# Performance work log

Hardware: AMD Instinct MI355X
Metric: run time of the kernel (lower is better)

The kernel has to match this reference:

```python
import jax, jax.numpy as jnp
import numpy as np

H = 1024
E = 8
TOP_K = 2


def setup_inputs() -> dict:
    key = jax.random.key(0)
    ks = jax.random.split(key, 6)
    B, S = 4, 2048
    hidden_states = jax.random.normal(ks[0], (B, S, H), dtype=jnp.float32)
    # router weight, init N(0, 0.02)
    router_w = jax.random.normal(ks[1], (E, H), dtype=jnp.float32) * 0.02
    # stacked expert FFN params (nn.Linear: y = x @ W.T + b)
    lim = 1.0 / np.sqrt(H)
    W1 = jax.random.uniform(ks[2], (E, H, H), minval=-lim, maxval=lim, dtype=jnp.float32)
    b1 = jax.random.uniform(ks[3], (E, H), minval=-lim, maxval=lim, dtype=jnp.float32)
    W2 = jax.random.uniform(ks[4], (E, H, H), minval=-lim, maxval=lim, dtype=jnp.float32)
    b2 = jax.random.uniform(ks[5], (E, H), minval=-lim, maxval=lim, dtype=jnp.float32)
    return {"hidden_states": hidden_states, "router_w": router_w,
            "W1": W1, "b1": b1, "W2": W2, "b2": b2}


def reference(hidden_states, router_w, W1, b1, W2, b2):
    B, S, _ = hidden_states.shape
    # ---- router ----
    logits = jnp.einsum('bsh,eh->bse', hidden_states, router_w)  # [B,S,E]
    router_probs = jax.nn.softmax(logits.astype(jnp.float32), axis=-1)
    top_vals, top_idx = jax.lax.top_k(router_probs, TOP_K)        # [B,S,K]
    top_vals = top_vals / jnp.sum(top_vals, axis=-1, keepdims=True)  # norm_topk_prob
    # per-token per-expert combine weight (sum of top-k weights matching expert)
    w = jnp.sum(jax.nn.one_hot(top_idx, E, dtype=top_vals.dtype) * top_vals[..., None], axis=-2)  # [B,S,E]
    # ---- dense all-expert FFN (faithful to reference: every expert on every token) ----
    h1 = jax.nn.relu(jnp.einsum('bsh,efh->bsef', hidden_states, W1) + b1)   # [B,S,E,F]
    expert_out = jnp.einsum('bsef,egf->bseg', h1, W2) + b2                  # [B,S,E,H]
    moe_out = jnp.einsum('bseh,bse->bsh', expert_out, w)
    return hidden_states + moe_out, router_probs
```

## Files before the change

kernel.cpp:

```cpp
#include <hip/hip_runtime.h>
#include <hip/hip_bf16.h>


#define HD   1024
#define NTOK 8192
#define NEXP 8
#define BM   128
#define BN   128
#define BK   32
#define ZROW 8192
#define MAXP 17408
#define EP_LDSW 136

typedef __attribute__((ext_vector_type(8))) short  vshort8;
typedef __attribute__((ext_vector_type(4))) short  vshort4;
typedef __attribute__((ext_vector_type(4))) float  vfloat4;

typedef __attribute__((address_space(1))) const unsigned gas_uint;
typedef __attribute__((address_space(3))) unsigned       las_uint;

__device__ __forceinline__ void gld16(const void* g, void* l) {
    __builtin_amdgcn_global_load_lds((gas_uint*)g, (las_uint*)l, 16, 0, 0);
}

__device__ __forceinline__ short bf16r(float f) {
    union { float f; unsigned u; } a; a.f = f;
    unsigned r = a.u + 0x7FFFu + ((a.u >> 16) & 1u);
    return (short)(r >> 16);
}

__global__ void init_kernel(int* counts, int* fill, int* pair_token, short* xb) {
    int i = blockIdx.x * 256 + threadIdx.x;
    if (i < NEXP) { counts[i] = 0; fill[i] = 0; }
    if (i < MAXP) pair_token[i] = ZROW;
    if (i < HD / 8) {
        vshort8 z = {0, 0, 0, 0, 0, 0, 0, 0};
        *(vshort8*)(xb + (size_t)ZROW * HD + i * 8) = z;
    }
}

__global__ __launch_bounds__(256) void router_kernel(
    const float* __restrict__ x, const float* __restrict__ rw,
    float* __restrict__ out, short* __restrict__ xb,
    float* __restrict__ probs_out, int2* __restrict__ tok_top,
    float2* __restrict__ tok_w, int* __restrict__ counts) {
    __shared__ float rws[NEXP * HD];
    __shared__ int hist[NEXP];
    int t = threadIdx.x;
    if (t < NEXP) hist[t] = 0;
    for (int j = 0; j < 8; ++j) {
        int idx = j * 1024 + t * 4;
        *(vfloat4*)(rws + idx) = *(const vfloat4*)(rw + idx);
    }
    __syncthreads();
    int wave = t >> 6, lane = t & 63;
    for (int it = 0; it < 8; ++it) {
        int token = blockIdx.x * 32 + it * 4 + wave;
        const float* xr = x + (size_t)token * HD;
        float part[NEXP];
#pragma unroll
        for (int e = 0; e < NEXP; ++e) part[e] = 0.f;
        for (int j = 0; j < 4; ++j) {
            int off = j * 256 + lane * 4;
            vfloat4 xv = *(const vfloat4*)(xr + off);
            *(vfloat4*)(out + (size_t)token * HD + off) = xv;
            vshort4 bq;
            bq.x = bf16r(xv.x); bq.y = bf16r(xv.y); bq.z = bf16r(xv.z); bq.w = bf16r(xv.w);
            *(vshort4*)(xb + (size_t)token * HD + off) = bq;
#pragma unroll
            for (int e = 0; e < NEXP; ++e) {
                vfloat4 wv = *(const vfloat4*)(rws + e * HD + off);
                part[e] += xv.x * wv.x + xv.y * wv.y + xv.z * wv.z + xv.w * wv.w;
            }
        }
#pragma unroll
        for (int e = 0; e < NEXP; ++e)
            for (int off = 32; off; off >>= 1)
                part[e] += __shfl_xor(part[e], off, 64);
        if (lane == 0) {
            float m = part[0];
#pragma unroll
            for (int e = 1; e < NEXP; ++e) m = fmaxf(m, part[e]);
            float p[NEXP], s = 0.f;
#pragma unroll
            for (int e = 0; e < NEXP; ++e) { p[e] = expf(part[e] - m); s += p[e]; }
            float inv = 1.f / s;
#pragma unroll
            for (int e = 0; e < NEXP; ++e) {
                p[e] *= inv;
                probs_out[(size_t)token * NEXP + e] = p[e];
            }
            int i0 = 0;
#pragma unroll
            for (int e = 1; e < NEXP; ++e) if (p[e] > p[i0]) i0 = e;
            int i1 = (i0 == 0) ? 1 : 0;
#pragma unroll
            for (int e = 0; e < NEXP; ++e) if (e != i0 && p[e] > p[i1]) i1 = e;
            float s2 = 1.f / (p[i0] + p[i1]);
            tok_top[token] = make_int2(i0, i1);
            tok_w[token]   = make_float2(p[i0] * s2, p[i1] * s2);
            atomicAdd(&hist[i0], 1);
            atomicAdd(&hist[i1], 1);
        }
    }
    __syncthreads();
    if (t < NEXP) atomicAdd(&counts[t], hist[t]);
}

__global__ __launch_bounds__(256) void scatter_kernel(
    const int2* __restrict__ tok_top, const float2* __restrict__ tok_w,
    const int* __restrict__ counts, int* fill,
    int* __restrict__ pair_token, float* __restrict__ pair_w) {
    __shared__ int lhist[NEXP];
    __shared__ int lbase[NEXP];
    int t = threadIdx.x;
    if (t < NEXP) lhist[t] = 0;
    __syncthreads();
    int offs[NEXP];
    {
        int acc = 0;
#pragma unroll
        for (int f = 0; f < NEXP; ++f) {
            offs[f] = acc;
            acc += (counts[f] + 127) & ~127;
        }
    }
    int token = blockIdx.x * 256 + t;
    int2 ti = tok_top[token];
    float2 tw = tok_w[token];
    int r0 = atomicAdd(&lhist[ti.x], 1);
    int r1 = atomicAdd(&lhist[ti.y], 1);
    __syncthreads();
    if (t < NEXP) lbase[t] = atomicAdd(&fill[t], lhist[t]);
    __syncthreads();
    int s0 = offs[ti.x] + lbase[ti.x] + r0;
    pair_token[s0] = token; pair_w[s0] = tw.x;
    int s1 = offs[ti.y] + lbase[ti.y] + r1;
    pair_token[s1] = token; pair_w[s1] = tw.y;
}

__global__ void convw_kernel(const float* __restrict__ W1, const float* __restrict__ W2,
                             short* __restrict__ D1, short* __restrict__ D2) {
    size_t t = (size_t)blockIdx.x * 256 + threadIdx.x;
    const size_t PER = (size_t)NEXP * HD * HD / 8;
    const float* src = W1; short* dst = D1;
    if (t >= PER) { t -= PER; src = W2; dst = D2; }
    size_t C = t >> 6;
    int l  = (int)(t & 63);
    int kc = (int)(C & 31);
    int ng = (int)((C >> 5) & 63);
    int ei = (int)(C >> 11);
    int n = ng * 16 + (l & 15);
    int k = kc * 32 + (l >> 4) * 8;
    const float* s = src + ((size_t)ei * HD + n) * HD + k;
    vfloat4 a = *(const vfloat4*)s;
    vfloat4 b = *(const vfloat4*)(s + 4);
    vshort8 o;
    o[0] = bf16r(a.x); o[1] = bf16r(a.y); o[2] = bf16r(a.z); o[3] = bf16r(a.w);
    o[4] = bf16r(b.x); o[5] = bf16r(b.y); o[6] = bf16r(b.z); o[7] = bf16r(b.w);
    *(vshort8*)(dst + t * 8) = o;
}

template <int MODE>
__global__ __launch_bounds__(512, 8) void moe_gemm(
    const short* __restrict__ A, const short* __restrict__ Bw,
    const float* __restrict__ bias, const int* __restrict__ pair_token,
    const float* __restrict__ pair_w, const int* __restrict__ counts,
    short* __restrict__ h1sw_out, float* __restrict__ out) {
    __shared__ short smem[16384];

    const int row0 = blockIdx.x * BM;
    int e = 0;
    {
        int csum = 0;
#pragma unroll
        for (int f = 0; f < NEXP; ++f) {
            int p = (counts[f] + 127) & ~127;
            if (csum + p <= row0) e = f + 1;
            csum += p;
        }
        if (row0 >= csum) return;
    }

    const int t = threadIdx.x;
    const int wave = t >> 6, lane = t & 63;
    const int wm = wave >> 2, wn = wave & 3;
    const int quad = lane >> 4, l16 = lane & 15;
    const int colb = blockIdx.y * BN;

    const char* agp;
    if (MODE == 0) {
        int tok = pair_token[row0 + wave * 16 + l16];
        agp = (const char*)A + (size_t)tok * (HD * 2) + quad * 16;
    } else {
        agp = (const char*)A + ((size_t)(row0 >> 4) + wave) * 32768 + lane * 16;
    }
    const char* bgp = (const char*)Bw +
        ((size_t)e * 64 + (colb >> 4) + wave) * 32768 + lane * 16;

    vfloat4 acc[4][2];
#pragma unroll
    for (int i = 0; i < 4; ++i)
#pragma unroll
        for (int j = 0; j < 2; ++j)
            acc[i][j] = (vfloat4){0.f, 0.f, 0.f, 0.f};

#define STAGE(bsel, kt_)                                                      \
    {                                                                         \
        const char* ga_ = (MODE == 0) ? (agp + (size_t)(kt_) * 64)            \
                                      : (agp + (size_t)(kt_) * 1024);         \
        gld16(ga_, smem + (bsel) * 4096 + wave * 512);                        \
        gld16(bgp + (size_t)(kt_) * 1024,                                     \
              smem + 8192 + (bsel) * 4096 + wave * 512);                      \
    }

    STAGE(0, 0)
    int cur = 0;
    for (int kt = 0; kt < HD / BK; ++kt) {
        if (kt < HD / BK - 1) {
            STAGE(cur ^ 1, kt + 1)
            asm volatile("s_waitcnt vmcnt(2)" ::: "memory");
        } else {
            asm volatile("s_waitcnt vmcnt(0)" ::: "memory");
        }
        __builtin_amdgcn_s_barrier();
        asm volatile("" ::: "memory");
        const short* sa = smem + cur * 4096;
        const short* sb = smem + 8192 + cur * 4096;
        vshort8 af[4], bfr[2];
#pragma unroll
        for (int i = 0; i < 4; ++i)
            af[i] = *(const vshort8*)(sa + (wm * 4 + i) * 512 + lane * 8);
#pragma unroll
        for (int j = 0; j < 2; ++j)
            bfr[j] = *(const vshort8*)(sb + (wn * 2 + j) * 512 + lane * 8);
#pragma unroll
        for (int i = 0; i < 4; ++i)
#pragma unroll
            for (int j = 0; j < 2; ++j)
                acc[i][j] = __builtin_amdgcn_mfma_f32_16x16x32_bf16(af[i], bfr[j], acc[i][j], 0, 0, 0);
        asm volatile("" ::: "memory");
        __builtin_amdgcn_s_barrier();
        cur ^= 1;
    }
#undef STAGE

    if (MODE == 0) {
        __syncthreads();
#pragma unroll
        for (int p = 0; p < 2; ++p) {
            if (wm == p) {
#pragma unroll
                for (int j = 0; j < 2; ++j) {
                    int col = wn * 32 + j * 16 + l16;
                    float bv = bias[e * HD + colb + col];
#pragma unroll
                    for (int i = 0; i < 4; ++i) {
                        int rl = i * 16 + quad * 4;
#pragma unroll
                        for (int reg = 0; reg < 4; ++reg) {
                            float v = acc[i][j][reg] + bv;
                            v = v > 0.f ? v : 0.f;
                            smem[(rl + reg) * EP_LDSW + col] = bf16r(v);
                        }
                    }
                }
            }
            __syncthreads();
#pragma unroll
            for (int c = 0; c < 2; ++c) {
                int idx = wave * 2 + c;
                int rg = idx >> 2, kc = idx & 3;
                vshort8 v = *(const vshort8*)(smem + (rg * 16 + l16) * EP_LDSW + kc * 32 + quad * 8);
                size_t chunk = ((size_t)(row0 >> 4) + p * 4 + rg) * 32 + (colb >> 5) + kc;
                *(vshort8*)(h1sw_out + chunk * 512 + lane * 8) = v;
            }
            if (p == 0) __syncthreads();
        }
    } else {
        int tok[4][4]; float wv[4][4];
#pragma unroll
        for (int i = 0; i < 4; ++i)
#pragma unroll
            for (int reg = 0; reg < 4; ++reg) {
                int r = row0 + wm * 64 + i * 16 + quad * 4 + reg;
                tok[i][reg] = pair_token[r];
                wv[i][reg] = pair_w[r];
            }
#pragma unroll
        for (int j = 0; j < 2; ++j) {
            int col = colb + wn * 32 + j * 16 + l16;
            float bv = bias[e * HD + col];
#pragma unroll
            for (int i = 0; i < 4; ++i)
#pragma unroll
                for (int reg = 0; reg < 4; ++reg)
                    if (tok[i][reg] < ZROW)
                        atomicAdd(out + (size_t)tok[i][reg] * HD + col,
                                  wv[i][reg] * (acc[i][j][reg] + bv));
        }
    }
}

extern "C" void kernel_launch(void* const* d_in, const int* in_sizes, int n_in,
                              void* d_out, int out_size, void* d_ws, size_t ws_size,
                              hipStream_t stream) {
    const float* x  = (const float*)d_in[0];
    const float* rw = (const float*)d_in[1];
    const float* W1 = (const float*)d_in[2];
    const float* b1 = (const float*)d_in[3];
    const float* W2 = (const float*)d_in[4];
    const float* b2 = (const float*)d_in[5];
    float* out   = (float*)d_out;
    float* probs = out + (size_t)NTOK * HD;

    char* ws = (char*)d_ws;
    short* xb = (short*)ws;            ws += (size_t)(NTOK + 1) * HD * 2;
    short* h1 = (short*)ws;            ws += (size_t)MAXP * HD * 2;
    int*   pair_token = (int*)ws;      ws += MAXP * 4;
    float* pair_w     = (float*)ws;    ws += MAXP * 4;
    int*   counts = (int*)ws;          ws += 256;
    int*   fill   = (int*)ws;          ws += 256;
    int2*   tok_top = (int2*)ws;       ws += NTOK * 8;
    float2* tok_w   = (float2*)ws;     ws += NTOK * 8;
    short* w1sw = (short*)ws;          ws += (size_t)NEXP * HD * HD * 2;
    short* w2sw = (short*)ws;          ws += (size_t)NEXP * HD * HD * 2;
    (void)ws_size;

    init_kernel<<<MAXP / 256, 256, 0, stream>>>(counts, fill, pair_token, xb);
    router_kernel<<<NTOK / 32, 256, 0, stream>>>(x, rw, out, xb, probs,
                                                 tok_top, tok_w, counts);
    scatter_kernel<<<NTOK / 256, 256, 0, stream>>>(tok_top, tok_w, counts, fill,
                                                   pair_token, pair_w);
    int cg = (int)(2 * ((size_t)NEXP * HD * HD / 8) / 256);
    convw_kernel<<<cg, 256, 0, stream>>>(W1, W2, w1sw, w2sw);
    dim3 gg(MAXP / BM, HD / BN);
    moe_gemm<0><<<gg, 512, 0, stream>>>(xb, w1sw, b1, pair_token, pair_w, counts, h1, nullptr);
    moe_gemm<1><<<gg, 512, 0, stream>>>(h1, w2sw, b2, pair_token, pair_w, counts, nullptr, out);
}
```

Measured before the change: 339.2 us.

## Pre-gather routed tokens into MFMA-swizzled buffer and use 4-wave 64x64 warp tiles

```diff
diff --git a/kernel.cpp b/kernel.cpp
--- a/kernel.cpp
+++ b/kernel.cpp
@@ -29,19 +29,15 @@
     return (short)(r >> 16);
 }
 
-__global__ void init_kernel(int* counts, int* fill, int* pair_token, short* xb) {
+__global__ void init_kernel(int* counts, int* fill, int* pair_token) {
     int i = blockIdx.x * 256 + threadIdx.x;
     if (i < NEXP) { counts[i] = 0; fill[i] = 0; }
     if (i < MAXP) pair_token[i] = ZROW;
-    if (i < HD / 8) {
-        vshort8 z = {0, 0, 0, 0, 0, 0, 0, 0};
-        *(vshort8*)(xb + (size_t)ZROW * HD + i * 8) = z;
-    }
 }
 
 __global__ __launch_bounds__(256) void router_kernel(
     const float* __restrict__ x, const float* __restrict__ rw,
-    float* __restrict__ out, short* __restrict__ xb,
+    float* __restrict__ out,
     float* __restrict__ probs_out, int2* __restrict__ tok_top,
     float2* __restrict__ tok_w, int* __restrict__ counts) {
     __shared__ float rws[NEXP * HD];
@@ -64,9 +60,6 @@
             int off = j * 256 + lane * 4;
             vfloat4 xv = *(const vfloat4*)(xr + off);
             *(vfloat4*)(out + (size_t)token * HD + off) = xv;
-            vshort4 bq;
-            bq.x = bf16r(xv.x); bq.y = bf16r(xv.y); bq.z = bf16r(xv.z); bq.w = bf16r(xv.w);
-            *(vshort4*)(xb + (size_t)token * HD + off) = bq;
 #pragma unroll
             for (int e = 0; e < NEXP; ++e) {
                 vfloat4 wv = *(const vfloat4*)(rws + e * HD + off);
@@ -161,8 +154,27 @@
     *(vshort8*)(dst + t * 8) = o;
 }
 
+__global__ __launch_bounds__(256) void gather_kernel(
+    const float* __restrict__ x, const int* __restrict__ pair_token,
+    short* __restrict__ xg) {
+    int id = blockIdx.x * 256 + threadIdx.x;
+    int C = id >> 6, l = id & 63;
+    int slot = ((C >> 5) << 4) + (l & 15);
+    int k = (C & 31) * 32 + (l >> 4) * 8;
+    int tok = pair_token[slot];
+    vshort8 o = {0, 0, 0, 0, 0, 0, 0, 0};
+    if (tok < ZROW) {
+        const float* s = x + (size_t)tok * HD + k;
+        vfloat4 a = *(const vfloat4*)s;
+        vfloat4 b = *(const vfloat4*)(s + 4);
+        o[0] = bf16r(a.x); o[1] = bf16r(a.y); o[2] = bf16r(a.z); o[3] = bf16r(a.w);
+        o[4] = bf16r(b.x); o[5] = bf16r(b.y); o[6] = bf16r(b.z); o[7] = bf16r(b.w);
+    }
+    *(vshort8*)(xg + (size_t)id * 8) = o;
+}
+
 template <int MODE>
-__global__ __launch_bounds__(512, 8) void moe_gemm(
+__global__ __launch_bounds__(256, 3) void moe_gemm(
     const short* __restrict__ A, const short* __restrict__ Bw,
     const float* __restrict__ bias, const int* __restrict__ pair_token,
     const float* __restrict__ pair_w, const int* __restrict__ counts,
@@ -184,34 +196,32 @@
 
     const int t = threadIdx.x;
     const int wave = t >> 6, lane = t & 63;
-    const int wm = wave >> 2, wn = wave & 3;
+    const int wm = wave >> 1, wn = wave & 1;
     const int quad = lane >> 4, l16 = lane & 15;
     const int colb = blockIdx.y * BN;
 
-    const char* agp;
-    if (MODE == 0) {
-        int tok = pair_token[row0 + wave * 16 + l16];
-        agp = (const char*)A + (size_t)tok * (HD * 2) + quad * 16;
-    } else {
-        agp = (const char*)A + ((size_t)(row0 >> 4) + wave) * 32768 + lane * 16;
-    }
-    const char* bgp = (const char*)Bw +
-        ((size_t)e * 64 + (colb >> 4) + wave) * 32768 + lane * 16;
-
-    vfloat4 acc[4][2];
+    const char* agp0 = (const char*)A +
+        ((size_t)(row0 >> 4) + 2 * wave) * 32768 + lane * 16;
+    const char* agp1 = agp0 + 32768;
+    const char* bgp0 = (const char*)Bw +
+        ((size_t)e * 64 + (colb >> 4) + 2 * wave) * 32768 + lane * 16;
+    const char* bgp1 = bgp0 + 32768;
+
+    vfloat4 acc[4][4];
 #pragma unroll
     for (int i = 0; i < 4; ++i)
 #pragma unroll
-        for (int j = 0; j < 2; ++j)
+        for (int j = 0; j < 4; ++j)
             acc[i][j] = (vfloat4){0.f, 0.f, 0.f, 0.f};
 
 #define STAGE(bsel, kt_)                                                      \
     {                                                                         \
-        const char* ga_ = (MODE == 0) ? (agp + (size_t)(kt_) * 64)            \
-                                      : (agp + (size_t)(kt_) * 1024);         \
-        gld16(ga_, smem + (bsel) * 4096 + wave * 512);                        \
-        gld16(bgp + (size_t)(kt_) * 1024,                                     \
-              smem + 8192 + (bsel) * 4096 + wave * 512);                      \
+        short* sa_ = smem + (bsel) * 4096;                                    \
+        short* sb_ = smem + 8192 + (bsel) * 4096;                             \
+        gld16(agp0 + (size_t)(kt_) * 1024, sa_ + (2 * wave) * 512);           \
+        gld16(agp1 + (size_t)(kt_) * 1024, sa_ + (2 * wave + 1) * 512);       \
+        gld16(bgp0 + (size_t)(kt_) * 1024, sb_ + (2 * wave) * 512);           \
+        gld16(bgp1 + (size_t)(kt_) * 1024, sb_ + (2 * wave + 1) * 512);       \
     }
 
     STAGE(0, 0)
@@ -219,7 +229,7 @@
     for (int kt = 0; kt < HD / BK; ++kt) {
         if (kt < HD / BK - 1) {
             STAGE(cur ^ 1, kt + 1)
-            asm volatile("s_waitcnt vmcnt(2)" ::: "memory");
+            asm volatile("s_waitcnt vmcnt(4)" ::: "memory");
         } else {
             asm volatile("s_waitcnt vmcnt(0)" ::: "memory");
         }
@@ -227,17 +237,17 @@
         asm volatile("" ::: "memory");
         const short* sa = smem + cur * 4096;
         const short* sb = smem + 8192 + cur * 4096;
-        vshort8 af[4], bfr[2];
+        vshort8 af[4], bfr[4];
 #pragma unroll
         for (int i = 0; i < 4; ++i)
             af[i] = *(const vshort8*)(sa + (wm * 4 + i) * 512 + lane * 8);
 #pragma unroll
-        for (int j = 0; j < 2; ++j)
-            bfr[j] = *(const vshort8*)(sb + (wn * 2 + j) * 512 + lane * 8);
+        for (int j = 0; j < 4; ++j)
+            bfr[j] = *(const vshort8*)(sb + (wn * 4 + j) * 512 + lane * 8);
 #pragma unroll
         for (int i = 0; i < 4; ++i)
 #pragma unroll
-            for (int j = 0; j < 2; ++j)
+            for (int j = 0; j < 4; ++j)
                 acc[i][j] = __builtin_amdgcn_mfma_f32_16x16x32_bf16(af[i], bfr[j], acc[i][j], 0, 0, 0);
         asm volatile("" ::: "memory");
         __builtin_amdgcn_s_barrier();
@@ -251,8 +261,8 @@
         for (int p = 0; p < 2; ++p) {
             if (wm == p) {
 #pragma unroll
-                for (int j = 0; j < 2; ++j) {
-                    int col = wn * 32 + j * 16 + l16;
+                for (int j = 0; j < 4; ++j) {
+                    int col = wn * 64 + j * 16 + l16;
                     float bv = bias[e * HD + colb + col];
 #pragma unroll
                     for (int i = 0; i < 4; ++i) {
@@ -268,8 +278,8 @@
             }
             __syncthreads();
 #pragma unroll
-            for (int c = 0; c < 2; ++c) {
-                int idx = wave * 2 + c;
+            for (int c = 0; c < 4; ++c) {
+                int idx = wave * 4 + c;
                 int rg = idx >> 2, kc = idx & 3;
                 vshort8 v = *(const vshort8*)(smem + (rg * 16 + l16) * EP_LDSW + kc * 32 + quad * 8);
                 size_t chunk = ((size_t)(row0 >> 4) + p * 4 + rg) * 32 + (colb >> 5) + kc;
@@ -288,8 +298,8 @@
                 wv[i][reg] = pair_w[r];
             }
 #pragma unroll
-        for (int j = 0; j < 2; ++j) {
-            int col = colb + wn * 32 + j * 16 + l16;
+        for (int j = 0; j < 4; ++j) {
+            int col = colb + wn * 64 + j * 16 + l16;
             float bv = bias[e * HD + col];
 #pragma unroll
             for (int i = 0; i < 4; ++i)
@@ -315,7 +325,7 @@
     float* probs = out + (size_t)NTOK * HD;
 
     char* ws = (char*)d_ws;
-    short* xb = (short*)ws;            ws += (size_t)(NTOK + 1) * HD * 2;
+    short* xg = (short*)ws;            ws += (size_t)MAXP * HD * 2;
     short* h1 = (short*)ws;            ws += (size_t)MAXP * HD * 2;
     int*   pair_token = (int*)ws;      ws += MAXP * 4;
     float* pair_w     = (float*)ws;    ws += MAXP * 4;
@@ -327,14 +337,15 @@
     short* w2sw = (short*)ws;          ws += (size_t)NEXP * HD * HD * 2;
     (void)ws_size;
 
-    init_kernel<<<MAXP / 256, 256, 0, stream>>>(counts, fill, pair_token, xb);
-    router_kernel<<<NTOK / 32, 256, 0, stream>>>(x, rw, out, xb, probs,
+    init_kernel<<<MAXP / 256, 256, 0, stream>>>(counts, fill, pair_token);
+    router_kernel<<<NTOK / 32, 256, 0, stream>>>(x, rw, out, probs,
                                                  tok_top, tok_w, counts);
     scatter_kernel<<<NTOK / 256, 256, 0, stream>>>(tok_top, tok_w, counts, fill,
                                                    pair_token, pair_w);
     int cg = (int)(2 * ((size_t)NEXP * HD * HD / 8) / 256);
     convw_kernel<<<cg, 256, 0, stream>>>(W1, W2, w1sw, w2sw);
+    gather_kernel<<<(MAXP * HD / 8) / 256, 256, 0, stream>>>(x, pair_token, xg);
     dim3 gg(MAXP / BM, HD / BN);
-    moe_gemm<0><<<gg, 512, 0, stream>>>(xb, w1sw, b1, pair_token, pair_w, counts, h1, nullptr);
-    moe_gemm<1><<<gg, 512, 0, stream>>>(h1, w2sw, b2, pair_token, pair_w, counts, nullptr, out);
-}
+    moe_gemm<0><<<gg, 256, 0, stream>>>(xg, w1sw, b1, pair_token, pair_w, counts, h1, nullptr);
+    moe_gemm<1><<<gg, 256, 0, stream>>>(h1, w2sw, b2, pair_token, pair_w, counts, nullptr, out);
+}
```

Result: no change. 339.7 us (+0.1%).
